# Kernel optimization log

Measured on AMD Instinct MI355X. Metric: run time of the kernel, lower is better.

Reference implementation:

```python
import jax, jax.numpy as jnp
import numpy as np

N = 100000        # nodes
E = 3200000       # random edges (avg degree 32); self-loops added in reference
IN, HID, HEADS, OUT = 10, 32, 2, 4
NEG_SLOPE = 0.2   # PyG GATConv default leaky_relu slope


def setup_inputs() -> dict:
    key = jax.random.key(0)
    ks = jax.random.split(key, 16)
    s = 0.1
    return {
        "x": jax.random.normal(ks[0], (N, IN), jnp.float32),
        "edge_index": jax.random.randint(ks[1], (2, E), 0, N),
        "W1": jax.random.normal(ks[2], (IN, HEADS * HID), jnp.float32) * s,
        "a1s": jax.random.normal(ks[3], (HEADS, HID), jnp.float32) * s,
        "a1d": jax.random.normal(ks[4], (HEADS, HID), jnp.float32) * s,
        "b1": jnp.zeros((HEADS * HID,), jnp.float32),
        "W2": jax.random.normal(ks[5], (HEADS * HID, HEADS * HID), jnp.float32) * s,
        "a2s": jax.random.normal(ks[6], (HEADS, HID), jnp.float32) * s,
        "a2d": jax.random.normal(ks[7], (HEADS, HID), jnp.float32) * s,
        "b2": jnp.zeros((HEADS * HID,), jnp.float32),
        "W3": jax.random.normal(ks[8], (HEADS * HID, OUT), jnp.float32) * s,
        "a3s": jax.random.normal(ks[9], (1, OUT), jnp.float32) * s,
        "a3d": jax.random.normal(ks[10], (1, OUT), jnp.float32) * s,
        "b3": jnp.zeros((OUT,), jnp.float32),
    }


def gat_layer(x, src, dst, W, a_src, a_dst, b, concat):
    """One PyG-style GATConv (shared src/dst linear, self-loops already in src/dst)."""
    heads, oc = a_src.shape
    h = (x @ W).reshape(-1, heads, oc)                    # [N, H, C]
    asc = jnp.einsum('nhc,hc->nh', h, a_src)              # [N, H]
    adc = jnp.einsum('nhc,hc->nh', h, a_dst)              # [N, H]
    e = jax.nn.leaky_relu(asc[src] + adc[dst], NEG_SLOPE) # [Etot, H]
    m = jax.ops.segment_max(e, dst, num_segments=N)       # segment softmax over dst
    ex = jnp.exp(e - m[dst])
    z = jax.ops.segment_sum(ex, dst, num_segments=N)
    alpha = ex / z[dst]                                   # [Etot, H]
    out = jax.ops.segment_sum(h[src] * alpha[:, :, None], dst, num_segments=N)
    out = out.reshape(-1, heads * oc) if concat else out.mean(axis=1)
    return out + b


def reference(x, edge_index, W1, a1s, a1d, b1, W2, a2s, a2d, b2, W3, a3s, a3d, b3):
    loops = jnp.arange(N)
    src = jnp.concatenate([edge_index[0], loops])
    dst = jnp.concatenate([edge_index[1], loops])
    h = jax.nn.relu(gat_layer(x, src, dst, W1, a1s, a1d, b1, True))
    h = jax.nn.relu(gat_layer(h, src, dst, W2, a2s, a2d, b2, True))
    h = gat_layer(h, src, dst, W3, a3s, a3d, b3, False)
    return jax.nn.sigmoid(h) * 100.0
```

## Files before the change

kernel.cpp:

```cpp
#include <hip/hip_runtime.h>
#include <hip/hip_bf16.h>
#include <math.h>

#define NEG_SLOPE 0.2f
#define PSHIFT 8
#define PSIZE 256
#define NPARTS_MAX 392
#define B1 768
#define CELL_CAP 32
#define PCAP 10240
#define LCSR_CAP 10240

typedef int vint2 __attribute__((ext_vector_type(2)));
typedef int vint4 __attribute__((ext_vector_type(4)));
typedef short bf16x8 __attribute__((ext_vector_type(8)));
typedef float floatx4 __attribute__((ext_vector_type(4)));

__device__ __forceinline__ float lrelu(float v) { return fmaxf(v, NEG_SLOPE * v); }

__device__ __forceinline__ unsigned short f2bf(float f) {
    unsigned int b = __float_as_uint(f);
    b += 0x7fffu + ((b >> 16) & 1u);
    return (unsigned short)(b >> 16);
}
__device__ __forceinline__ float bf2f(unsigned short u) {
    return __uint_as_float((unsigned int)u << 16);
}

__global__ void k_part(const int* __restrict__ src, const int* __restrict__ dst, int E,
                       int* __restrict__ pairs, int* __restrict__ ptot, int nparts) {
    __shared__ int stage[NPARTS_MAX * CELL_CAP];
    __shared__ int lcnt[NPARTS_MAX];
    int tid = threadIdx.x, blk = blockIdx.x;
    for (int i = tid; i < nparts; i += 256) lcnt[i] = 0;
    __syncthreads();
    int per = ((E + B1 * 4 - 1) / (B1 * 4)) * 4;
    int s = blk * per, e = min(E, s + per);
    bool al = ((E & 3) == 0);
    for (int i0 = s + tid * 4; i0 < e; i0 += 1024) {
        int dv[4], sv[4], nv;
        if (al && i0 + 4 <= e) {
            vint4 d4 = __builtin_nontemporal_load((const vint4*)(dst + i0));
            vint4 s4 = __builtin_nontemporal_load((const vint4*)(src + i0));
            dv[0] = d4.x; dv[1] = d4.y; dv[2] = d4.z; dv[3] = d4.w;
            sv[0] = s4.x; sv[1] = s4.y; sv[2] = s4.z; sv[3] = s4.w;
            nv = 4;
        } else {
            nv = min(4, e - i0);
            for (int k = 0; k < nv; ++k) {
                dv[k] = __builtin_nontemporal_load(dst + i0 + k);
                sv[k] = __builtin_nontemporal_load(src + i0 + k);
            }
        }
        for (int k = 0; k < nv; ++k) {
            int p = dv[k] >> PSHIFT;
            int pos = atomicAdd(&lcnt[p], 1);
            if (pos < CELL_CAP)
                stage[p * CELL_CAP + pos] = (sv[k] << PSHIFT) | (dv[k] & (PSIZE - 1));
        }
    }
    __syncthreads();
    for (int p = tid; p < nparts; p += 256) {
        int tgt = min(lcnt[p], CELL_CAP);
        if (tgt == 0) continue;
        int base = atomicAdd(&ptot[p], tgt);
        if (base + tgt > PCAP) tgt = max(0, PCAP - base);
        int* gp = pairs + (size_t)p * PCAP + base;
        const int* sp = &stage[p * CELL_CAP];
        for (int j = 0; j < tgt; ++j) gp[j] = sp[j];
    }
}

__global__ void k_pscan(const int* __restrict__ ptot, int* __restrict__ pbase,
                        int* __restrict__ row, int nparts, int N) {
    __shared__ int sh[512];
    int tid = threadIdx.x;
    int v = (tid < nparts) ? min(ptot[tid], PCAP) : 0;
    sh[tid] = v;
    __syncthreads();
    for (int off = 1; off < 512; off <<= 1) {
        int t = (tid >= off) ? sh[tid - off] : 0;
        __syncthreads();
        sh[tid] += t;
        __syncthreads();
    }
    if (tid < nparts) pbase[tid] = sh[tid] - v;
    if (tid == nparts - 1) row[N] = sh[tid];
}

__global__ void k_scat2(const int* __restrict__ pairs, const int* __restrict__ ptot,
                        const int* __restrict__ pbase, int* __restrict__ row,
                        int* __restrict__ csr, int N) {
    __shared__ int lcsr[LCSR_CAP];
    __shared__ int lhist[PSIZE], lcur[PSIZE];
    int part = blockIdx.x;
    int lo = part << PSHIFT;
    int npart = min(PSIZE, N - lo);
    int tid = threadIdx.x;
    int cnt = min(ptot[part], PCAP);
    const int* seg = pairs + (size_t)part * PCAP;
    for (int i = tid; i < PSIZE; i += 1024) lhist[i] = 0;
    __syncthreads();
    for (int i = tid; i < cnt; i += 1024)
        atomicAdd(&lhist[__builtin_nontemporal_load(&seg[i]) & (PSIZE - 1)], 1);
    __syncthreads();
    if (tid < PSIZE) lcur[tid] = lhist[tid];
    __syncthreads();
    for (int off = 1; off < PSIZE; off <<= 1) {
        int t = 0;
        if (tid < PSIZE && tid >= off) t = lcur[tid - off];
        __syncthreads();
        if (tid < PSIZE) lcur[tid] += t;
        __syncthreads();
    }
    int pb = pbase[part];
    if (tid < npart) row[lo + tid] = pb + lcur[tid] - lhist[tid];
    if (tid < PSIZE) lcur[tid] -= lhist[tid];
    __syncthreads();
    for (int i = tid; i < cnt; i += 1024) {
        int v = __builtin_nontemporal_load(&seg[i]);
        int pos = atomicAdd(&lcur[v & (PSIZE - 1)], 1);
        if (pos < LCSR_CAP) lcsr[pos] = (unsigned)v >> PSHIFT;
    }
    __syncthreads();
    for (int i = tid; i < cnt; i += 1024)
        csr[pb + i] = lcsr[i];
}

__global__ void k_lin1(const float* __restrict__ x, const float* __restrict__ W,
                       const float* __restrict__ as_, const float* __restrict__ ad_,
                       unsigned short* __restrict__ hb, float* __restrict__ asc,
                       float* __restrict__ adc, int N) {
    __shared__ float sW[10 * 64];
    int tid = threadIdx.x;
    for (int i = tid; i < 640; i += 256) sW[i] = W[i];
    __syncthreads();
    int wid = tid >> 6, lane = tid & 63;
    int n = blockIdx.x * 4 + wid;
    if (n >= N) return;
    float acc = 0.f;
#pragma unroll
    for (int k = 0; k < 10; ++k) acc += x[n * 10 + k] * sW[k * 64 + lane];
    hb[(size_t)n * 64 + lane] = f2bf(acc);
    int head = lane >> 5, cc = lane & 31;
    float rs = acc * as_[lane];
    float rd = acc * ad_[lane];
#pragma unroll
    for (int m = 16; m >= 1; m >>= 1) {
        rs += __shfl_xor(rs, m, 64);
        rd += __shfl_xor(rd, m, 64);
    }
    if (cc == 0) { asc[n * 2 + head] = rs; adc[n * 2 + head] = rd; }
}

__global__ void k_lin2(const float* __restrict__ yin, const float* __restrict__ W,
                       const float* __restrict__ as_, const float* __restrict__ ad_,
                       unsigned short* __restrict__ hb, float* __restrict__ asc,
                       float* __restrict__ adc, int N) {
    __shared__ unsigned short sW[64 * 64];
    int tid = threadIdx.x;
    for (int i = tid; i < 4096; i += 256) sW[i] = f2bf(W[i]);
    __syncthreads();
    int wid = tid >> 6, lane = tid & 63;
    int quad = lane >> 4, col = lane & 15;
    bf16x8 bfr[4][2];
#pragma unroll
    for (int blk = 0; blk < 4; ++blk)
#pragma unroll
        for (int kh = 0; kh < 2; ++kh)
#pragma unroll
            for (int j = 0; j < 8; ++j)
                bfr[blk][kh][j] = (short)sW[(kh * 32 + quad * 8 + j) * 64 + blk * 16 + col];
    float asv[4], adv[4];
#pragma unroll
    for (int blk = 0; blk < 4; ++blk) {
        asv[blk] = as_[blk * 16 + col];
        adv[blk] = ad_[blk * 16 + col];
    }
    int tile = blockIdx.x * 4 + wid;
    int nb = tile * 16;
    if (nb >= N) return;
    int mrow = nb + col; if (mrow >= N) mrow = N - 1;
    const float* yr = yin + (size_t)mrow * 64;
    bf16x8 afr[2];
#pragma unroll
    for (int kh = 0; kh < 2; ++kh) {
        const float4* p = (const float4*)(yr + kh * 32 + quad * 8);
        float4 u0 = p[0], u1 = p[1];
        afr[kh][0] = (short)f2bf(u0.x); afr[kh][1] = (short)f2bf(u0.y);
        afr[kh][2] = (short)f2bf(u0.z); afr[kh][3] = (short)f2bf(u0.w);
        afr[kh][4] = (short)f2bf(u1.x); afr[kh][5] = (short)f2bf(u1.y);
        afr[kh][6] = (short)f2bf(u1.z); afr[kh][7] = (short)f2bf(u1.w);
    }
    floatx4 acc[4];
#pragma unroll
    for (int blk = 0; blk < 4; ++blk) {
        acc[blk][0] = 0.f; acc[blk][1] = 0.f; acc[blk][2] = 0.f; acc[blk][3] = 0.f;
        acc[blk] = __builtin_amdgcn_mfma_f32_16x16x32_bf16(afr[0], bfr[blk][0], acc[blk], 0, 0, 0);
        acc[blk] = __builtin_amdgcn_mfma_f32_16x16x32_bf16(afr[1], bfr[blk][1], acc[blk], 0, 0, 0);
    }
#pragma unroll
    for (int r = 0; r < 4; ++r) {
        int m = nb + quad * 4 + r;
        if (m < N) {
#pragma unroll
            for (int blk = 0; blk < 4; ++blk)
                hb[(size_t)m * 64 + blk * 16 + col] = f2bf(acc[blk][r]);
        }
    }
    float s0[4], s1[4], d0[4], d1[4];
#pragma unroll
    for (int r = 0; r < 4; ++r) {
        s0[r] = acc[0][r] * asv[0] + acc[1][r] * asv[1];
        s1[r] = acc[2][r] * asv[2] + acc[3][r] * asv[3];
        d0[r] = acc[0][r] * adv[0] + acc[1][r] * adv[1];
        d1[r] = acc[2][r] * adv[2] + acc[3][r] * adv[3];
    }
#pragma unroll
    for (int mask = 8; mask >= 1; mask >>= 1) {
#pragma unroll
        for (int r = 0; r < 4; ++r) {
            s0[r] += __shfl_xor(s0[r], mask, 64);
            s1[r] += __shfl_xor(s1[r], mask, 64);
            d0[r] += __shfl_xor(d0[r], mask, 64);
            d1[r] += __shfl_xor(d1[r], mask, 64);
        }
    }
    if (col < 4) {
        int m = nb + quad * 4 + col;
        if (m < N) {
            float vs0 = col == 0 ? s0[0] : col == 1 ? s0[1] : col == 2 ? s0[2] : s0[3];
            float vs1 = col == 0 ? s1[0] : col == 1 ? s1[1] : col == 2 ? s1[2] : s1[3];
            float vd0 = col == 0 ? d0[0] : col == 1 ? d0[1] : col == 2 ? d0[2] : d0[3];
            float vd1 = col == 0 ? d1[0] : col == 1 ? d1[1] : col == 2 ? d1[2] : d1[3];
            asc[m * 2 + 0] = vs0; asc[m * 2 + 1] = vs1;
            adc[m * 2 + 0] = vd0; adc[m * 2 + 1] = vd1;
        }
    }
}

__global__ void k_agg(const unsigned short* __restrict__ hb, const float* __restrict__ asc,
                      const float* __restrict__ adc, const int* __restrict__ row,
                      const int* __restrict__ csr_src, const float* __restrict__ bias,
                      float* __restrict__ yout, int N, int do_relu) {
    __shared__ vint2 tbl[4][64];
    int tid = threadIdx.x;
    int wid = tid >> 6, lane = tid & 63;
    int n = blockIdx.x * 4 + wid;
    if (n >= N) return;
    int s = row[n], e = row[n + 1];
    int head = lane >> 5, sub = lane & 31;
    int chq = lane & 15;
    int hq = chq >> 3;
    int jo = lane >> 4;
    float2 ad = ((const float2*)adc)[n];
    float adch = head ? ad.y : ad.x;
    float2 asf = ((const float2*)asc)[n];
    float p_self_h = __expf(lrelu((head ? asf.y : asf.x) + adch));
    float zl = (sub == 0) ? p_self_h : 0.f;
    float a0 = 0.f, a1 = 0.f, a2 = 0.f, a3 = 0.f;
    const vint2* hb64 = (const vint2*)hb;
    for (int base = s; base < e; base += 32) {
        int cnt = e - base; if (cnt > 32) cnt = 32;
        int idx = base + sub;
        int srcv = 0;
        float p_l = 0.f;
        if (idx < e) {
            srcv = csr_src[idx];
            p_l = __expf(lrelu(asc[(size_t)srcv * 2 + head] + adch));
        }
        zl += p_l;
        vint2 ent; ent.x = srcv; ent.y = __float_as_int(p_l);
        tbl[wid][(head << 5) | sub] = ent;
        __builtin_amdgcn_wave_barrier();
        int tb = hq << 5;
#pragma unroll 4
        for (int j = jo; j < cnt; j += 4) {
            vint2 t = tbl[wid][tb | j];
            vint2 pk = hb64[(size_t)t.x * 16 + chq];
            float p = __int_as_float(t.y);
            unsigned int pa = (unsigned int)pk.x, pb = (unsigned int)pk.y;
            a0 += p * __uint_as_float(pa << 16);
            a1 += p * __uint_as_float(pa & 0xffff0000u);
            a2 += p * __uint_as_float(pb << 16);
            a3 += p * __uint_as_float(pb & 0xffff0000u);
        }
        __builtin_amdgcn_wave_barrier();
    }
    a0 += __shfl_xor(a0, 16, 64); a1 += __shfl_xor(a1, 16, 64);
    a2 += __shfl_xor(a2, 16, 64); a3 += __shfl_xor(a3, 16, 64);
    a0 += __shfl_xor(a0, 32, 64); a1 += __shfl_xor(a1, 32, 64);
    a2 += __shfl_xor(a2, 32, 64); a3 += __shfl_xor(a3, 32, 64);
#pragma unroll
    for (int msk = 16; msk >= 1; msk >>= 1) zl += __shfl_xor(zl, msk, 64);
    float zo = __shfl_xor(zl, 32, 64);
    float zneed = (hq == head) ? zl : zo;
    float adcm = hq ? ad.y : ad.x;
    float p_self_my = __expf(lrelu((hq ? asf.y : asf.x) + adcm));
    vint2 pks = hb64[(size_t)n * 16 + chq];
    unsigned int sa = (unsigned int)pks.x, sb = (unsigned int)pks.y;
    a0 += p_self_my * __uint_as_float(sa << 16);
    a1 += p_self_my * __uint_as_float(sa & 0xffff0000u);
    a2 += p_self_my * __uint_as_float(sb << 16);
    a3 += p_self_my * __uint_as_float(sb & 0xffff0000u);
    float inv = 1.f / zneed;
    float4 bv = ((const float4*)bias)[chq];
    float y0 = a0 * inv + bv.x;
    float y1 = a1 * inv + bv.y;
    float y2 = a2 * inv + bv.z;
    float y3 = a3 * inv + bv.w;
    if (do_relu) {
        y0 = fmaxf(y0, 0.f); y1 = fmaxf(y1, 0.f);
        y2 = fmaxf(y2, 0.f); y3 = fmaxf(y3, 0.f);
    }
    if (lane < 16) {
        float4 o; o.x = y0; o.y = y1; o.z = y2; o.w = y3;
        ((float4*)yout)[(size_t)n * 16 + chq] = o;
    }
}

__global__ void k_lin3(const float* __restrict__ yin, const float* __restrict__ W3,
                       const float* __restrict__ a3s, const float* __restrict__ a3d,
                       float4* __restrict__ rec, int N) {
    __shared__ float sW[256];
    int tid = threadIdx.x;
    sW[tid] = W3[tid];
    __syncthreads();
    int t = blockIdx.x * 256 + tid;
    int n = t >> 2, c = t & 3;
    if (n >= N) return;
    float acc = 0.f;
#pragma unroll
    for (int k = 0; k < 64; ++k) acc += yin[(size_t)n * 64 + k] * sW[k * 4 + c];
    float rs = acc * a3s[c], rd = acc * a3d[c];
    rs += __shfl_xor(rs, 1, 64); rs += __shfl_xor(rs, 2, 64);
    rd += __shfl_xor(rd, 1, 64); rd += __shfl_xor(rd, 2, 64);
    float a_1 = __shfl_xor(acc, 1, 64);
    float a_2 = __shfl_xor(acc, 2, 64);
    float a_3 = __shfl_xor(acc, 3, 64);
    if (c == 0) {
        unsigned int lo = (unsigned int)f2bf(acc) | ((unsigned int)f2bf(a_1) << 16);
        unsigned int hi = (unsigned int)f2bf(a_2) | ((unsigned int)f2bf(a_3) << 16);
        float4 r;
        r.x = __uint_as_float(lo); r.y = __uint_as_float(hi);
        r.z = rs; r.w = rd;
        rec[n] = r;
    }
}

__global__ void k_agg3(const float4* __restrict__ rec, const int* __restrict__ row,
                       const int* __restrict__ csr_src, const float* __restrict__ b3,
                       float* __restrict__ out, int N) {
    int tid = threadIdx.x;
    int wid = tid >> 6, lane = tid & 63;
    int n = blockIdx.x * 4 + wid;
    if (n >= N) return;
    int s = row[n], e = row[n + 1];
    float4 rn = rec[n];
    float adcn = rn.w;
    float n0 = 0.f, n1 = 0.f, n2 = 0.f, n3 = 0.f, den = 0.f;
    if (lane == 0) {
        float p = __expf(lrelu(rn.z + adcn));
        unsigned int lo = __float_as_uint(rn.x), hi = __float_as_uint(rn.y);
        n0 = p * __uint_as_float(lo << 16);
        n1 = p * __uint_as_float(lo & 0xffff0000u);
        n2 = p * __uint_as_float(hi << 16);
        n3 = p * __uint_as_float(hi & 0xffff0000u);
        den = p;
    }
    for (int idx = s + lane; idx < e; idx += 64) {
        int src = csr_src[idx];
        float4 r = rec[src];
        float p = __expf(lrelu(r.z + adcn));
        unsigned int lo = __float_as_uint(r.x), hi = __float_as_uint(r.y);
        n0 += p * __uint_as_float(lo << 16);
        n1 += p * __uint_as_float(lo & 0xffff0000u);
        n2 += p * __uint_as_float(hi << 16);
        n3 += p * __uint_as_float(hi & 0xffff0000u);
        den += p;
    }
#pragma unroll
    for (int msk = 32; msk >= 1; msk >>= 1) {
        n0 += __shfl_xor(n0, msk, 64);
        n1 += __shfl_xor(n1, msk, 64);
        n2 += __shfl_xor(n2, msk, 64);
        n3 += __shfl_xor(n3, msk, 64);
        den += __shfl_xor(den, msk, 64);
    }
    if (lane < 4) {
        float num = lane == 0 ? n0 : lane == 1 ? n1 : lane == 2 ? n2 : n3;
        float v = num / den + b3[lane];
        out[n * 4 + lane] = 100.f / (1.f + __expf(-v));
    }
}

extern "C" void kernel_launch(void* const* d_in, const int* in_sizes, int n_in,
                              void* d_out, int out_size, void* d_ws, size_t ws_size,
                              hipStream_t stream) {
    const float* x   = (const float*)d_in[0];
    const int*   ei  = (const int*)d_in[1];
    const float* W1  = (const float*)d_in[2];
    const float* a1s = (const float*)d_in[3];
    const float* a1d = (const float*)d_in[4];
    const float* b1  = (const float*)d_in[5];
    const float* W2  = (const float*)d_in[6];
    const float* a2s = (const float*)d_in[7];
    const float* a2d = (const float*)d_in[8];
    const float* b2  = (const float*)d_in[9];
    const float* W3  = (const float*)d_in[10];
    const float* a3s = (const float*)d_in[11];
    const float* a3d = (const float*)d_in[12];
    const float* b3  = (const float*)d_in[13];
    float* out = (float*)d_out;

    const int N = in_sizes[0] / 10;
    const int E = in_sizes[1] / 2;
    const int* esrc = ei;
    const int* edst = ei + E;
    const int nparts = (N + PSIZE - 1) >> PSHIFT;

    char* ws = (char*)d_ws;
    size_t off = 0;
    auto alloc = [&](size_t bytes) {
        void* p = ws + off;
        off = (off + bytes + 255) & ~(size_t)255;
        return p;
    };
    int*   row   = (int*)alloc((size_t)(N + 1) * sizeof(int));
    int*   ptot  = (int*)alloc(NPARTS_MAX * sizeof(int));
    int*   pbase = (int*)alloc(NPARTS_MAX * sizeof(int));
    int*   csr   = (int*)alloc((size_t)E * sizeof(int));
    unsigned short* hb = (unsigned short*)alloc((size_t)N * 64 * sizeof(unsigned short));
    float* y     = (float*)alloc((size_t)N * 64 * sizeof(float));
    float4* rec  = (float4*)alloc((size_t)N * sizeof(float4));
    float* asc   = (float*)alloc((size_t)N * 2 * sizeof(float));
    float* adc   = (float*)alloc((size_t)N * 2 * sizeof(float));
    int* pairs = (int*)hb;

    (void)hipMemsetAsync(ptot, 0, NPARTS_MAX * sizeof(int), stream);

    const int nw = (N + 3) / 4;
    const int tiles = (N + 15) / 16;

    k_part<<<B1, 256, 0, stream>>>(esrc, edst, E, pairs, ptot, nparts);
    k_pscan<<<1, 512, 0, stream>>>(ptot, pbase, row, nparts, N);
    k_scat2<<<nparts, 1024, 0, stream>>>(pairs, ptot, pbase, row, csr, N);

    k_lin1<<<nw, 256, 0, stream>>>(x, W1, a1s, a1d, hb, asc, adc, N);
    k_agg<<<nw, 256, 0, stream>>>(hb, asc, adc, row, csr, b1, y, N, 1);
    k_lin2<<<(tiles + 3) / 4, 256, 0, stream>>>(y, W2, a2s, a2d, hb, asc, adc, N);
    k_agg<<<nw, 256, 0, stream>>>(hb, asc, adc, row, csr, b2, y, N, 1);
    k_lin3<<<(N * 4 + 255) / 256, 256, 0, stream>>>(y, W3, a3s, a3d, rec, N);
    k_agg3<<<nw, 256, 0, stream>>>(rec, row, csr, b3, out, N);
}
```

Baseline: 364.6 us.

## Widen GAT aggregation gathers to 16B and process 64-edge chunks; half-wave agg3

The layer-1/2 aggregation kernel now gathers each neighbor's bf16 features with 16-byte loads, 8 lanes per row, so 8 edges are in flight per wave. It also stages 64 edges per chunk in shared memory and precomputes byte offsets (src<<7) to save address arithmetic. The final-layer aggregation assigns one node per 32-lane half-wave instead of a full wave, which should waste fewer lanes at an average degree of about 33. In exchange each lane holds more accumulators, which raises register pressure, and the reduction needs more shuffle steps.

```diff
diff --git a/kernel.cpp b/kernel.cpp
--- a/kernel.cpp
+++ b/kernel.cpp
@@ -10,6 +10,7 @@
 #define CELL_CAP 32
 #define PCAP 10240
 #define LCSR_CAP 10240
+#define CHUNK 64
 
 typedef int vint2 __attribute__((ext_vector_type(2)));
 typedef int vint4 __attribute__((ext_vector_type(4)));
@@ -243,79 +244,110 @@
                       const float* __restrict__ adc, const int* __restrict__ row,
                       const int* __restrict__ csr_src, const float* __restrict__ bias,
                       float* __restrict__ yout, int N, int do_relu) {
-    __shared__ vint2 tbl[4][64];
+    __shared__ vint2 tbl[4][2 * CHUNK];
     int tid = threadIdx.x;
     int wid = tid >> 6, lane = tid & 63;
     int n = blockIdx.x * 4 + wid;
     if (n >= N) return;
     int s = row[n], e = row[n + 1];
     int head = lane >> 5, sub = lane & 31;
-    int chq = lane & 15;
-    int hq = chq >> 3;
-    int jo = lane >> 4;
+    int cho = lane & 7;
+    int hq = (lane >> 2) & 1;
+    int jo = lane >> 3;
+    int cho16 = cho << 4;
     float2 ad = ((const float2*)adc)[n];
     float adch = head ? ad.y : ad.x;
     float2 asf = ((const float2*)asc)[n];
     float p_self_h = __expf(lrelu((head ? asf.y : asf.x) + adch));
     float zl = (sub == 0) ? p_self_h : 0.f;
     float a0 = 0.f, a1 = 0.f, a2 = 0.f, a3 = 0.f;
-    const vint2* hb64 = (const vint2*)hb;
-    for (int base = s; base < e; base += 32) {
-        int cnt = e - base; if (cnt > 32) cnt = 32;
-        int idx = base + sub;
-        int srcv = 0;
-        float p_l = 0.f;
-        if (idx < e) {
-            srcv = csr_src[idx];
-            p_l = __expf(lrelu(asc[(size_t)srcv * 2 + head] + adch));
-        }
-        zl += p_l;
-        vint2 ent; ent.x = srcv; ent.y = __float_as_int(p_l);
-        tbl[wid][(head << 5) | sub] = ent;
+    float a4 = 0.f, a5 = 0.f, a6 = 0.f, a7 = 0.f;
+    const char* hbB = (const char*)hb;
+    vint2* mytbl = tbl[wid];
+    int tb = hq << 6;
+    int wbase = head << 6;
+    for (int base = s; base < e; base += CHUNK) {
+        int cnt = e - base; if (cnt > CHUNK) cnt = CHUNK;
+#pragma unroll
+        for (int h2 = 0; h2 < 2; ++h2) {
+            int idx = base + sub + h2 * 32;
+            int srcv = 0;
+            float p_l = 0.f;
+            if (idx < e) {
+                srcv = csr_src[idx];
+                p_l = __expf(lrelu(asc[(size_t)srcv * 2 + head] + adch));
+            }
+            zl += p_l;
+            vint2 ent; ent.x = srcv << 7; ent.y = __float_as_int(p_l);
+            mytbl[wbase | (sub + h2 * 32)] = ent;
+        }
         __builtin_amdgcn_wave_barrier();
-        int tb = hq << 5;
 #pragma unroll 4
-        for (int j = jo; j < cnt; j += 4) {
-            vint2 t = tbl[wid][tb | j];
-            vint2 pk = hb64[(size_t)t.x * 16 + chq];
+        for (int j = jo; j < cnt; j += 8) {
+            vint2 t = mytbl[tb | j];
+            vint4 pk = *(const vint4*)(hbB + (unsigned)(t.x | cho16));
             float p = __int_as_float(t.y);
-            unsigned int pa = (unsigned int)pk.x, pb = (unsigned int)pk.y;
-            a0 += p * __uint_as_float(pa << 16);
-            a1 += p * __uint_as_float(pa & 0xffff0000u);
-            a2 += p * __uint_as_float(pb << 16);
-            a3 += p * __uint_as_float(pb & 0xffff0000u);
+            unsigned int w0 = (unsigned int)pk.x, w1 = (unsigned int)pk.y;
+            unsigned int w2 = (unsigned int)pk.z, w3 = (unsigned int)pk.w;
+            a0 += p * __uint_as_float(w0 << 16);
+            a1 += p * __uint_as_float(w0 & 0xffff0000u);
+            a2 += p * __uint_as_float(w1 << 16);
+            a3 += p * __uint_as_float(w1 & 0xffff0000u);
+            a4 += p * __uint_as_float(w2 << 16);
+            a5 += p * __uint_as_float(w2 & 0xffff0000u);
+            a6 += p * __uint_as_float(w3 << 16);
+            a7 += p * __uint_as_float(w3 & 0xffff0000u);
         }
         __builtin_amdgcn_wave_barrier();
     }
-    a0 += __shfl_xor(a0, 16, 64); a1 += __shfl_xor(a1, 16, 64);
-    a2 += __shfl_xor(a2, 16, 64); a3 += __shfl_xor(a3, 16, 64);
-    a0 += __shfl_xor(a0, 32, 64); a1 += __shfl_xor(a1, 32, 64);
-    a2 += __shfl_xor(a2, 32, 64); a3 += __shfl_xor(a3, 32, 64);
+#pragma unroll
+    for (int msk = 8; msk <= 32; msk <<= 1) {
+        a0 += __shfl_xor(a0, msk, 64); a1 += __shfl_xor(a1, msk, 64);
+        a2 += __shfl_xor(a2, msk, 64); a3 += __shfl_xor(a3, msk, 64);
+        a4 += __shfl_xor(a4, msk, 64); a5 += __shfl_xor(a5, msk, 64);
+        a6 += __shfl_xor(a6, msk, 64); a7 += __shfl_xor(a7, msk, 64);
+    }
 #pragma unroll
     for (int msk = 16; msk >= 1; msk >>= 1) zl += __shfl_xor(zl, msk, 64);
     float zo = __shfl_xor(zl, 32, 64);
     float zneed = (hq == head) ? zl : zo;
     float adcm = hq ? ad.y : ad.x;
     float p_self_my = __expf(lrelu((hq ? asf.y : asf.x) + adcm));
-    vint2 pks = hb64[(size_t)n * 16 + chq];
-    unsigned int sa = (unsigned int)pks.x, sb = (unsigned int)pks.y;
-    a0 += p_self_my * __uint_as_float(sa << 16);
-    a1 += p_self_my * __uint_as_float(sa & 0xffff0000u);
-    a2 += p_self_my * __uint_as_float(sb << 16);
-    a3 += p_self_my * __uint_as_float(sb & 0xffff0000u);
+    vint4 pks = *(const vint4*)(hbB + (((unsigned)n << 7) | (unsigned)cho16));
+    {
+        unsigned int w0 = (unsigned int)pks.x, w1 = (unsigned int)pks.y;
+        unsigned int w2 = (unsigned int)pks.z, w3 = (unsigned int)pks.w;
+        a0 += p_self_my * __uint_as_float(w0 << 16);
+        a1 += p_self_my * __uint_as_float(w0 & 0xffff0000u);
+        a2 += p_self_my * __uint_as_float(w1 << 16);
+        a3 += p_self_my * __uint_as_float(w1 & 0xffff0000u);
+        a4 += p_self_my * __uint_as_float(w2 << 16);
+        a5 += p_self_my * __uint_as_float(w2 & 0xffff0000u);
+        a6 += p_self_my * __uint_as_float(w3 << 16);
+        a7 += p_self_my * __uint_as_float(w3 & 0xffff0000u);
+    }
     float inv = 1.f / zneed;
-    float4 bv = ((const float4*)bias)[chq];
-    float y0 = a0 * inv + bv.x;
-    float y1 = a1 * inv + bv.y;
-    float y2 = a2 * inv + bv.z;
-    float y3 = a3 * inv + bv.w;
+    float4 bv0 = ((const float4*)bias)[cho * 2];
+    float4 bv1 = ((const float4*)bias)[cho * 2 + 1];
+    float y0 = a0 * inv + bv0.x;
+    float y1 = a1 * inv + bv0.y;
+    float y2 = a2 * inv + bv0.z;
+    float y3 = a3 * inv + bv0.w;
+    float y4 = a4 * inv + bv1.x;
+    float y5 = a5 * inv + bv1.y;
+    float y6 = a6 * inv + bv1.z;
+    float y7 = a7 * inv + bv1.w;
     if (do_relu) {
         y0 = fmaxf(y0, 0.f); y1 = fmaxf(y1, 0.f);
         y2 = fmaxf(y2, 0.f); y3 = fmaxf(y3, 0.f);
-    }
-    if (lane < 16) {
-        float4 o; o.x = y0; o.y = y1; o.z = y2; o.w = y3;
-        ((float4*)yout)[(size_t)n * 16 + chq] = o;
+        y4 = fmaxf(y4, 0.f); y5 = fmaxf(y5, 0.f);
+        y6 = fmaxf(y6, 0.f); y7 = fmaxf(y7, 0.f);
+    }
+    if (jo == 0) {
+        float4 o0; o0.x = y0; o0.y = y1; o0.z = y2; o0.w = y3;
+        float4 o1; o1.x = y4; o1.y = y5; o1.z = y6; o1.w = y7;
+        ((float4*)yout)[(size_t)n * 16 + cho * 2] = o0;
+        ((float4*)yout)[(size_t)n * 16 + cho * 2 + 1] = o1;
     }
 }
 
@@ -352,8 +384,8 @@
                        const int* __restrict__ csr_src, const float* __restrict__ b3,
                        float* __restrict__ out, int N) {
     int tid = threadIdx.x;
-    int wid = tid >> 6, lane = tid & 63;
-    int n = blockIdx.x * 4 + wid;
+    int half = tid >> 5, lane = tid & 31;
+    int n = blockIdx.x * 8 + half;
     if (n >= N) return;
     int s = row[n], e = row[n + 1];
     float4 rn = rec[n];
@@ -368,7 +400,7 @@
         n3 = p * __uint_as_float(hi & 0xffff0000u);
         den = p;
     }
-    for (int idx = s + lane; idx < e; idx += 64) {
+    for (int idx = s + lane; idx < e; idx += 32) {
         int src = csr_src[idx];
         float4 r = rec[src];
         float p = __expf(lrelu(r.z + adcn));
@@ -380,7 +412,7 @@
         den += p;
     }
 #pragma unroll
-    for (int msk = 32; msk >= 1; msk >>= 1) {
+    for (int msk = 16; msk >= 1; msk >>= 1) {
         n0 += __shfl_xor(n0, msk, 64);
         n1 += __shfl_xor(n1, msk, 64);
         n2 += __shfl_xor(n2, msk, 64);
@@ -451,5 +483,5 @@
     k_lin2<<<(tiles + 3) / 4, 256, 0, stream>>>(y, W2, a2s, a2d, hb, asc, adc, N);
     k_agg<<<nw, 256, 0, stream>>>(hb, asc, adc, row, csr, b2, y, N, 1);
     k_lin3<<<(N * 4 + 255) / 256, 256, 0, stream>>>(y, W3, a3s, a3d, rec, N);
-    k_agg3<<<nw, 256, 0, stream>>>(rec, row, csr, b3, out, N);
-}
+    k_agg3<<<(N + 7) / 8, 256, 0, stream>>>(rec, row, csr, b3, out, N);
+}
```

Measured after the change: 355.4 us. 2.5% less time.
